# Kernel tuning notes

Measured on AMD Instinct MI355X. Metric: run time of the kernel, lower is better.

## Reference

```python
import jax, jax.numpy as jnp
import numpy as np

B, S, D = 8, 2048, 128
NEG = -1e9

def setup_inputs() -> dict:
    key = jax.random.key(0)
    kq, kk, kv = jax.random.split(key, 3)
    query = jax.random.normal(kq, (B, S, D), dtype=jnp.float32)
    k_ = jax.random.normal(kk, (B, S, D), dtype=jnp.float32)
    value = jax.random.normal(kv, (B, S, D), dtype=jnp.float32)
    mask = jnp.tril(jnp.ones((S, S), dtype=jnp.int32))  # causal (seq_len, seq_len)
    return {"query": query, "key": k_, "value": value, "mask": mask}

def reference(query, key, value, mask):
    d_k = query.shape[-1]
    # scores: [B, S, S]
    scores = jnp.einsum('bqd,bkd->bqk', query, key) / jnp.sqrt(jnp.asarray(d_k, jnp.float32))
    scores = jnp.where(mask == 0, jnp.asarray(NEG, scores.dtype), scores)
    p_attn = jax.nn.softmax(scores, axis=-1)
    # dropout p=0.0 -> identity
    return jnp.einsum('bqk,bkd->bqd', p_attn, value)
```

## Files before the change

kernel.cpp:

```cpp
#include <hip/hip_runtime.h>


#define BATCH 8
#define SEQ   2048
#define DIM   128
#define CK    256

typedef _Float16 v4h __attribute__((ext_vector_type(4)));
typedef _Float16 v8h __attribute__((ext_vector_type(8)));
typedef float    v4f __attribute__((ext_vector_type(4)));

#define QF_H 0u
#define KF_H 2097152u
#define VF_H 4194304u
#define OP_H 6291456u
#define ML_B 31457280u
#define WS_NEED 31752192u

__constant__ const float kScale = 0.08838834764831845f;

__global__ __launch_bounds__(256) void prepass(
    const float* __restrict__ K, const float* __restrict__ V,
    _Float16* __restrict__ wsh)
{
    const int b = blockIdx.x;
    const int t = threadIdx.x;
    if (b < 1024) {
        __shared__ float tile[16][132];
        const int batch = b >> 7, vt = b & 127;
        const float* src = V + ((size_t)batch * SEQ + vt * 16) * DIM;
        const int row = t >> 4, col = (t & 15) * 8;
        *(v4f*)&tile[row][col]     = *(const v4f*)(src + (size_t)row * DIM + col);
        *(v4f*)&tile[row][col + 4] = *(const v4f*)(src + (size_t)row * DIM + col + 4);
        __syncthreads();
        const int n = t >> 4, p = (t >> 2) & 3, qd = t & 3;
        v8h h;
        #pragma unroll
        for (int j = 0; j < 8; ++j) {
            const int d  = 32 * p + 16 * (j >> 2) + n;
            const int kk = qd * 4 + (j & 3);
            h[j] = (_Float16)tile[kk][d];
        }
        const int w = n * 64 + ((p * 16 + qd * 4) ^ ((n & 7) << 2));
        *(v8h*)(wsh + VF_H + (size_t)batch * 262144 + vt * 2048 + w * 2) = h;
    } else {
        const int i = (b - 1024) * 256 + t;
        const int seg = i & 15, row = i >> 4;
        const float* src = K + (size_t)row * DIM + seg * 8;
        v4f a = *(const v4f*)src;
        v4f c = *(const v4f*)(src + 4);
        v8h h;
        #pragma unroll
        for (int j = 0; j < 4; ++j) {
            h[j]     = (_Float16)a[j];
            h[j + 4] = (_Float16)c[j];
        }
        const int w = (seg * 4) ^ ((row & 7) << 2);
        *(v8h*)(wsh + KF_H + (size_t)row * DIM + w * 2) = h;
    }
}

__device__ __forceinline__ void dma16(const _Float16* g, const _Float16* l) {
    __builtin_amdgcn_global_load_lds(
        (const __attribute__((address_space(1))) unsigned int*)g,
        (__attribute__((address_space(3))) unsigned int*)(unsigned int)(uintptr_t)l,
        16, 0, 0);
}

__global__ __launch_bounds__(256, 4) void attn_chunk(
    const float* __restrict__ Q, const _Float16* __restrict__ wsh,
    float* __restrict__ Ml, _Float16* __restrict__ Op)
{
    __shared__ __align__(16) _Float16 lds[16384];

    const int batch = blockIdx.x & 7;
    int g = blockIdx.x >> 3;
    int c = 0;
    for (; c < 8; ++c) { const int cnt = 32 - 4 * c; if (g < cnt) break; g -= cnt; }
    const int wave = threadIdx.x >> 6;
    const int qt = 16 * c + g * 4 + wave;
    const int q0 = qt * 16;
    const int kbeg = c * CK;

    const int lane = threadIdx.x & 63;
    const int n = lane & 15, quad = lane >> 4;
    const size_t bo = (size_t)batch * SEQ * DIM;

    const _Float16* Kf = wsh + KF_H + bo;
    const _Float16* Vf = wsh + VF_H + bo;

    v8h qa[4];
    {
        const float* qp = Q + bo + (size_t)(q0 + n) * DIM + quad * 8;
        #pragma unroll
        for (int p = 0; p < 4; ++p) {
            v4f a = *(const v4f*)(qp + p * 32);
            v4f b2 = *(const v4f*)(qp + p * 32 + 4);
            v8h h;
            #pragma unroll
            for (int j = 0; j < 4; ++j) {
                h[j]     = (_Float16)(a[j] * kScale);
                h[j + 4] = (_Float16)(b2[j] * kScale);
            }
            qa[p] = h;
        }
    }

    const _Float16* gseg = ((wave < 2) ? (Kf + (size_t)kbeg * DIM)
                                       : (Vf + (size_t)(kbeg >> 4) * 2048))
                           + (wave & 1) * 2048;
    const int ldsseg = (wave >> 1) * 4096 + (wave & 1) * 2048;

    int koff[4];
    #pragma unroll
    for (int p = 0; p < 4; ++p)
        koff[p] = n * 128 + (((quad * 4 + p * 16) ^ ((n & 7) << 2)) << 1);

    float l_run = 0.0f;
    v4f of[8];
    #pragma unroll
    for (int dc = 0; dc < 8; ++dc) of[dc] = (v4f){0.f, 0.f, 0.f, 0.f};

    const int qn0 = q0 + n - kbeg;
    const int kq = quad * 4;

    #pragma unroll
    for (int i = 0; i < 4; ++i)
        dma16(gseg + i * 512 + lane * 8, &lds[ldsseg + i * 512]);

    #pragma unroll
    for (int kb = 0; kb < 8; ++kb) {
        __syncthreads();
        if (kb < 7) {
            const _Float16* gs = gseg + (kb + 1) * 4096;
            const int lb = ((kb + 1) & 1) * 8192 + ldsseg;
            #pragma unroll
            for (int i = 0; i < 4; ++i)
                dma16(gs + i * 512 + lane * 8, &lds[lb + i * 512]);
        }
        const int base = (kb & 1) * 8192;
        #pragma unroll
        for (int t16 = 0; t16 < 2; ++t16) {
            v4f s = (v4f){0.f, 0.f, 0.f, 0.f};
            #pragma unroll
            for (int p = 0; p < 4; ++p) {
                v8h kf = *(const v8h*)&lds[base + t16 * 2048 + koff[p]];
                s = __builtin_amdgcn_mfma_f32_16x16x32_f16(kf, qa[p], s, 0, 0, 0);
            }
            v4h pf;
            float ps = 0.f;
            #pragma unroll
            for (int r = 0; r < 4; ++r) {
                const float sv = (kb * 32 + t16 * 16 + kq + r > qn0) ? -1e30f : s[r];
                const float p = __expf(sv);
                ps += p;
                pf[r] = (_Float16)p;
            }
            l_run += ps;
            #pragma unroll
            for (int p = 0; p < 4; ++p) {
                v8h vv = *(const v8h*)&lds[base + 4096 + t16 * 2048 + koff[p]];
                v4h vlo = __builtin_shufflevector(vv, vv, 0, 1, 2, 3);
                v4h vhi = __builtin_shufflevector(vv, vv, 4, 5, 6, 7);
                of[2 * p]     = __builtin_amdgcn_mfma_f32_16x16x16f16(vlo, pf, of[2 * p], 0, 0, 0);
                of[2 * p + 1] = __builtin_amdgcn_mfma_f32_16x16x16f16(vhi, pf, of[2 * p + 1], 0, 0, 0);
            }
        }
    }

    l_run += __shfl_xor(l_run, 16);
    l_run += __shfl_xor(l_run, 32);

    const int rs = (2048 * c - 128 * c * (c - 1)) * 8
                 + batch * (2048 - CK * c) + (q0 + n - CK * c);
    _Float16* op = (_Float16*)(wsh + OP_H) + (size_t)rs * DIM
                 - (size_t)0;
    op = Op + (size_t)rs * DIM;
    #pragma unroll
    for (int dc = 0; dc < 8; ++dc) {
        v4h o;
        #pragma unroll
        for (int r = 0; r < 4; ++r) o[r] = (_Float16)of[dc][r];
        *(v4h*)(op + dc * 16 + quad * 4) = o;
    }
    if (quad == 0) Ml[rs] = l_run;
}

__global__ __launch_bounds__(256) void combine(
    const _Float16* __restrict__ Op, const float* __restrict__ Ml,
    float* __restrict__ O)
{
    const int gid = blockIdx.x * 256 + threadIdx.x;
    const size_t e = (size_t)gid * 4;
    const int d = (int)(e & 127);
    const int q = (int)((e >> 7) & 2047);
    const int b = (int)(e >> 18);
    const int nc = (q >> 8) + 1;
    float L = 0.f;
    v4f acc = (v4f){0.f, 0.f, 0.f, 0.f};
    for (int c = 0; c < nc; ++c) {
        const int rs = (2048 * c - 128 * c * (c - 1)) * 8 + b * (2048 - 256 * c) + (q - 256 * c);
        L += Ml[rs];
        v4h o = *(const v4h*)(Op + (size_t)rs * DIM + d);
        #pragma unroll
        for (int r = 0; r < 4; ++r) acc[r] += (float)o[r];
    }
    const float rl = 1.0f / L;
    *(v4f*)(O + e) = acc * rl;
}

__global__ __launch_bounds__(128) void attn_fwd(
    const float* __restrict__ Q, const float* __restrict__ K,
    const float* __restrict__ V, float* __restrict__ O)
{
    const int batch = blockIdx.x & 7;
    const int qb    = blockIdx.x >> 3;
    const int tid   = threadIdx.x;
    const int wave  = tid >> 6;
    const int lane  = tid & 63;
    const int n     = lane & 15;
    const int quad  = lane >> 4;

    const int q0      = qb * 32 + wave * 16;
    const int my_last = qb * 2 + wave;
    const int nt      = qb * 2 + 2;

    const size_t bo = (size_t)batch * SEQ * DIM;

    __shared__ __align__(16) _Float16 Ks[16 * 136];
    __shared__ __align__(16) _Float16 Vt[128 * 20];
    typedef _Float16 v2h __attribute__((ext_vector_type(2)));

    v4h qf[8];
    {
        const float* qp = Q + bo + (size_t)(q0 + n) * DIM + quad * 4;
        #pragma unroll
        for (int dc = 0; dc < 8; ++dc) {
            v4f qv = *(const v4f*)(qp + dc * 16);
            v4h h;
            #pragma unroll
            for (int i = 0; i < 4; ++i) h[i] = (_Float16)(qv[i] * kScale);
            qf[dc] = h;
        }
    }

    float m_run = -1e30f, l_run = 0.0f;
    v4f of[8];
    #pragma unroll
    for (int dc = 0; dc < 8; ++dc) of[dc] = (v4f){0.f, 0.f, 0.f, 0.f};

    const int krow = tid >> 3;
    const int kcol = (tid & 7) * 16;
    const int vr   = (tid >> 4) * 2;
    const int vc   = (tid & 15) * 4;

    for (int tk = 0; tk < nt; ++tk) {
        const int k0 = tk * 16;
        {
            const float* kp = K + bo + (size_t)(k0 + krow) * DIM + kcol;
            v4f k0v = *(const v4f*)(kp);
            v4f k1v = *(const v4f*)(kp + 4);
            v4f k2v = *(const v4f*)(kp + 8);
            v4f k3v = *(const v4f*)(kp + 12);
            const float* vp = V + bo + (size_t)(k0 + vr) * DIM + vc;
            v4f va0 = *(const v4f*)(vp);
            v4f va1 = *(const v4f*)(vp + DIM);
            v4f vb0 = *(const v4f*)(vp + 64);
            v4f vb1 = *(const v4f*)(vp + DIM + 64);

            v8h h0, h1;
            #pragma unroll
            for (int i = 0; i < 4; ++i) {
                h0[i]     = (_Float16)k0v[i];
                h0[i + 4] = (_Float16)k1v[i];
                h1[i]     = (_Float16)k2v[i];
                h1[i + 4] = (_Float16)k3v[i];
            }
            *(v8h*)&Ks[krow * 136 + kcol]     = h0;
            *(v8h*)&Ks[krow * 136 + kcol + 8] = h1;

            #pragma unroll
            for (int i = 0; i < 4; ++i) {
                v2h p0 = { (_Float16)va0[i], (_Float16)va1[i] };
                v2h p1 = { (_Float16)vb0[i], (_Float16)vb1[i] };
                *(v2h*)&Vt[(vc + i) * 20 + vr]      = p0;
                *(v2h*)&Vt[(vc + 64 + i) * 20 + vr] = p1;
            }
        }
        __syncthreads();

        if (tk <= my_last) {
            v4f s = (v4f){0.f, 0.f, 0.f, 0.f};
            #pragma unroll
            for (int dc = 0; dc < 8; ++dc) {
                v4h kf = *(const v4h*)&Ks[n * 136 + dc * 16 + quad * 4];
                s = __builtin_amdgcn_mfma_f32_16x16x16f16(kf, qf[dc], s, 0, 0, 0);
            }
            if (tk == my_last) {
                #pragma unroll
                for (int r = 0; r < 4; ++r)
                    if (quad * 4 + r > n) s[r] = -1e30f;
            }
            float tm = fmaxf(fmaxf(s[0], s[1]), fmaxf(s[2], s[3]));
            tm = fmaxf(tm, __shfl_xor(tm, 16));
            tm = fmaxf(tm, __shfl_xor(tm, 32));
            const float m_new = fmaxf(m_run, tm);
            const float alpha = __expf(m_run - m_new);
            v4f p;
            #pragma unroll
            for (int r = 0; r < 4; ++r) p[r] = __expf(s[r] - m_new);
            float ps = p[0] + p[1] + p[2] + p[3];
            ps += __shfl_xor(ps, 16);
            ps += __shfl_xor(ps, 32);
            l_run = l_run * alpha + ps;
            m_run = m_new;

            v4h pf;
            #pragma unroll
            for (int r = 0; r < 4; ++r) pf[r] = (_Float16)p[r];

            #pragma unroll
            for (int dc = 0; dc < 8; ++dc) {
                v4h vf = *(const v4h*)&Vt[(dc * 16 + n) * 20 + quad * 4];
                of[dc] *= alpha;
                of[dc] = __builtin_amdgcn_mfma_f32_16x16x16f16(vf, pf, of[dc], 0, 0, 0);
            }
        }
        __syncthreads();
    }

    const float rl = 1.0f / l_run;
    float* op = O + bo + (size_t)(q0 + n) * DIM + quad * 4;
    #pragma unroll
    for (int dc = 0; dc < 8; ++dc) {
        v4f o = of[dc] * rl;
        *(v4f*)(op + dc * 16) = o;
    }
}

extern "C" void kernel_launch(void* const* d_in, const int* in_sizes, int n_in,
                              void* d_out, int out_size, void* d_ws, size_t ws_size,
                              hipStream_t stream) {
    const float* Q = (const float*)d_in[0];
    const float* K = (const float*)d_in[1];
    const float* V = (const float*)d_in[2];
    float* Out = (float*)d_out;

    if (ws_size >= (size_t)WS_NEED) {
        _Float16* wsh = (_Float16*)d_ws;
        _Float16* Op  = wsh + OP_H;
        float*    Ml  = (float*)((char*)d_ws + ML_B);
        prepass<<<dim3(2048), dim3(256), 0, stream>>>(K, V, wsh);
        attn_chunk<<<dim3(8 * 144), dim3(256), 0, stream>>>(Q, wsh, Ml, Op);
        combine<<<dim3(2048), dim3(256), 0, stream>>>(Op, Ml, Out);
    } else {
        attn_fwd<<<dim3(BATCH * (SEQ / 32)), dim3(128), 0, stream>>>(Q, K, V, Out);
    }
}
```

Baseline: 112.0 us.

## Fuse combine into chunk kernel via atomic last-block reduction and exp2

```diff
diff --git a/kernel.cpp b/kernel.cpp
--- a/kernel.cpp
+++ b/kernel.cpp
@@ -10,21 +10,23 @@
 typedef _Float16 v8h __attribute__((ext_vector_type(8)));
 typedef float    v4f __attribute__((ext_vector_type(4)));
 
-#define QF_H 0u
 #define KF_H 2097152u
 #define VF_H 4194304u
 #define OP_H 6291456u
 #define ML_B 31457280u
-#define WS_NEED 31752192u
-
-__constant__ const float kScale = 0.08838834764831845f;
+#define CNT_B 31752192u
+#define WS_NEED 31753216u
+
+__constant__ const float kScaleE2 = 0.12751744462783346f;
+__constant__ const float kScale   = 0.08838834764831845f;
 
 __global__ __launch_bounds__(256) void prepass(
     const float* __restrict__ K, const float* __restrict__ V,
-    _Float16* __restrict__ wsh)
+    _Float16* __restrict__ wsh, int* __restrict__ cnt)
 {
     const int b = blockIdx.x;
     const int t = threadIdx.x;
+    if (b == 0) cnt[t] = 0;
     if (b < 1024) {
         __shared__ float tile[16][132];
         const int batch = b >> 7, vt = b & 127;
@@ -69,18 +71,22 @@
 
 __global__ __launch_bounds__(256, 4) void attn_chunk(
     const float* __restrict__ Q, const _Float16* __restrict__ wsh,
-    float* __restrict__ Ml, _Float16* __restrict__ Op)
+    float* __restrict__ Ml, _Float16* __restrict__ Op,
+    int* __restrict__ cnt, float* __restrict__ O)
 {
     __shared__ __align__(16) _Float16 lds[16384];
+    __shared__ int sOld;
 
     const int batch = blockIdx.x & 7;
     int g = blockIdx.x >> 3;
     int c = 0;
-    for (; c < 8; ++c) { const int cnt = 32 - 4 * c; if (g < cnt) break; g -= cnt; }
+    for (; c < 8; ++c) { const int n4 = 32 - 4 * c; if (g < n4) break; g -= n4; }
     const int wave = threadIdx.x >> 6;
     const int qt = 16 * c + g * 4 + wave;
     const int q0 = qt * 16;
     const int kbeg = c * CK;
+    const int J = 4 * c + g;
+    const int nc = (J >> 2) + 1;
 
     const int lane = threadIdx.x & 63;
     const int n = lane & 15, quad = lane >> 4;
@@ -99,8 +105,8 @@
             v8h h;
             #pragma unroll
             for (int j = 0; j < 4; ++j) {
-                h[j]     = (_Float16)(a[j] * kScale);
-                h[j + 4] = (_Float16)(b2[j] * kScale);
+                h[j]     = (_Float16)(a[j] * kScaleE2);
+                h[j + 4] = (_Float16)(b2[j] * kScaleE2);
             }
             qa[p] = h;
         }
@@ -152,7 +158,7 @@
             #pragma unroll
             for (int r = 0; r < 4; ++r) {
                 const float sv = (kb * 32 + t16 * 16 + kq + r > qn0) ? -1e30f : s[r];
-                const float p = __expf(sv);
+                const float p = exp2f(sv);
                 ps += p;
                 pf[r] = (_Float16)p;
             }
@@ -171,11 +177,18 @@
     l_run += __shfl_xor(l_run, 16);
     l_run += __shfl_xor(l_run, 32);
 
+    if (nc == 1) {
+        const float rl = 1.0f / l_run;
+        float* Of = O + bo + (size_t)(q0 + n) * DIM;
+        #pragma unroll
+        for (int dc = 0; dc < 8; ++dc)
+            *(v4f*)(Of + dc * 16 + quad * 4) = of[dc] * rl;
+        return;
+    }
+
     const int rs = (2048 * c - 128 * c * (c - 1)) * 8
                  + batch * (2048 - CK * c) + (q0 + n - CK * c);
-    _Float16* op = (_Float16*)(wsh + OP_H) + (size_t)rs * DIM
-                 - (size_t)0;
-    op = Op + (size_t)rs * DIM;
+    _Float16* op = Op + (size_t)rs * DIM;
     #pragma unroll
     for (int dc = 0; dc < 8; ++dc) {
         v4h o;
@@ -184,29 +197,40 @@
         *(v4h*)(op + dc * 16 + quad * 4) = o;
     }
     if (quad == 0) Ml[rs] = l_run;
-}
-
-__global__ __launch_bounds__(256) void combine(
-    const _Float16* __restrict__ Op, const float* __restrict__ Ml,
-    float* __restrict__ O)
-{
-    const int gid = blockIdx.x * 256 + threadIdx.x;
-    const size_t e = (size_t)gid * 4;
-    const int d = (int)(e & 127);
-    const int q = (int)((e >> 7) & 2047);
-    const int b = (int)(e >> 18);
-    const int nc = (q >> 8) + 1;
-    float L = 0.f;
-    v4f acc = (v4f){0.f, 0.f, 0.f, 0.f};
-    for (int c = 0; c < nc; ++c) {
-        const int rs = (2048 * c - 128 * c * (c - 1)) * 8 + b * (2048 - 256 * c) + (q - 256 * c);
-        L += Ml[rs];
-        v4h o = *(const v4h*)(Op + (size_t)rs * DIM + d);
-        #pragma unroll
-        for (int r = 0; r < 4; ++r) acc[r] += (float)o[r];
-    }
-    const float rl = 1.0f / L;
-    *(v4f*)(O + e) = acc * rl;
+
+    __threadfence();
+    __syncthreads();
+    if (threadIdx.x == 0) sOld = atomicAdd(&cnt[batch * 32 + J], 1);
+    __syncthreads();
+    if (sOld == nc - 1) {
+        __threadfence();
+        const int t = threadIdx.x;
+        const int q = 64 * J + (t >> 2);
+        const int dseg = (t & 3) * 32;
+        float acc[32];
+        #pragma unroll
+        for (int x = 0; x < 32; ++x) acc[x] = 0.f;
+        float L = 0.f;
+        for (int cc = 0; cc < nc; ++cc) {
+            const int rr = (2048 * cc - 128 * cc * (cc - 1)) * 8
+                         + batch * (2048 - CK * cc) + (q - CK * cc);
+            L += Ml[rr];
+            const _Float16* pp = Op + (size_t)rr * DIM + dseg;
+            #pragma unroll
+            for (int j = 0; j < 4; ++j) {
+                v8h h = *(const v8h*)(pp + j * 8);
+                #pragma unroll
+                for (int x = 0; x < 8; ++x) acc[j * 8 + x] += (float)h[x];
+            }
+        }
+        const float rl = 1.0f / L;
+        float* Of = O + bo + (size_t)q * DIM + dseg;
+        #pragma unroll
+        for (int j = 0; j < 8; ++j) {
+            v4f o = { acc[j*4] * rl, acc[j*4+1] * rl, acc[j*4+2] * rl, acc[j*4+3] * rl };
+            *(v4f*)(Of + j * 4) = o;
+        }
+    }
 }
 
 __global__ __launch_bounds__(128) void attn_fwd(
@@ -350,9 +374,9 @@
         _Float16* wsh = (_Float16*)d_ws;
         _Float16* Op  = wsh + OP_H;
         float*    Ml  = (float*)((char*)d_ws + ML_B);
-        prepass<<<dim3(2048), dim3(256), 0, stream>>>(K, V, wsh);
-        attn_chunk<<<dim3(8 * 144), dim3(256), 0, stream>>>(Q, wsh, Ml, Op);
-        combine<<<dim3(2048), dim3(256), 0, stream>>>(Op, Ml, Out);
+        int*      cnt = (int*)((char*)d_ws + CNT_B);
+        prepass<<<dim3(2048), dim3(256), 0, stream>>>(K, V, wsh, cnt);
+        attn_chunk<<<dim3(8 * 144), dim3(256), 0, stream>>>(Q, wsh, Ml, Op, cnt, Out);
     } else {
         attn_fwd<<<dim3(BATCH * (SEQ / 32)), dim3(128), 0, stream>>>(Q, K, V, Out);
     }
```

Result: slower. 287.6 us (+156.7%).

## Process two query tiles per wave and write single-chunk rows directly

Applied to the files above, without the earlier changes.

```diff
diff --git a/kernel.cpp b/kernel.cpp
--- a/kernel.cpp
+++ b/kernel.cpp
@@ -10,14 +10,14 @@
 typedef _Float16 v8h __attribute__((ext_vector_type(8)));
 typedef float    v4f __attribute__((ext_vector_type(4)));
 
-#define QF_H 0u
 #define KF_H 2097152u
 #define VF_H 4194304u
 #define OP_H 6291456u
 #define ML_B 31457280u
 #define WS_NEED 31752192u
 
-__constant__ const float kScale = 0.08838834764831845f;
+__constant__ const float kScaleE2 = 0.12751744462783346f;
+__constant__ const float kScale   = 0.08838834764831845f;
 
 __global__ __launch_bounds__(256) void prepass(
     const float* __restrict__ K, const float* __restrict__ V,
@@ -33,7 +33,7 @@
         *(v4f*)&tile[row][col]     = *(const v4f*)(src + (size_t)row * DIM + col);
         *(v4f*)&tile[row][col + 4] = *(const v4f*)(src + (size_t)row * DIM + col + 4);
         __syncthreads();
-        const int n = t >> 4, p = (t >> 2) & 3, qd = t & 3;
+        const int n = t & 15, p = (t >> 4) & 3, qd = t >> 6;
         v8h h;
         #pragma unroll
         for (int j = 0; j < 8; ++j) {
@@ -67,20 +67,23 @@
         16, 0, 0);
 }
 
-__global__ __launch_bounds__(256, 4) void attn_chunk(
+__global__ __launch_bounds__(256, 3) void attn_chunk(
     const float* __restrict__ Q, const _Float16* __restrict__ wsh,
-    float* __restrict__ Ml, _Float16* __restrict__ Op)
+    float* __restrict__ Ml, _Float16* __restrict__ Op,
+    float* __restrict__ O)
 {
     __shared__ __align__(16) _Float16 lds[16384];
 
     const int batch = blockIdx.x & 7;
     int g = blockIdx.x >> 3;
     int c = 0;
-    for (; c < 8; ++c) { const int cnt = 32 - 4 * c; if (g < cnt) break; g -= cnt; }
+    for (; c < 8; ++c) { const int n8 = 16 - 2 * c; if (g < n8) break; g -= n8; }
     const int wave = threadIdx.x >> 6;
-    const int qt = 16 * c + g * 4 + wave;
-    const int q0 = qt * 16;
+    const int qtb = 16 * c + g * 8;
+    const int q0a = (qtb + 2 * wave) * 16;
+    const int q0b = q0a + 16;
     const int kbeg = c * CK;
+    const bool direct = (c == 0) && (g < 2);
 
     const int lane = threadIdx.x & 63;
     const int n = lane & 15, quad = lane >> 4;
@@ -89,20 +92,26 @@
     const _Float16* Kf = wsh + KF_H + bo;
     const _Float16* Vf = wsh + VF_H + bo;
 
-    v8h qa[4];
+    v8h qa[8];
     {
-        const float* qp = Q + bo + (size_t)(q0 + n) * DIM + quad * 8;
+        const float* qpa = Q + bo + (size_t)(q0a + n) * DIM + quad * 8;
+        const float* qpb = Q + bo + (size_t)(q0b + n) * DIM + quad * 8;
         #pragma unroll
         for (int p = 0; p < 4; ++p) {
-            v4f a = *(const v4f*)(qp + p * 32);
-            v4f b2 = *(const v4f*)(qp + p * 32 + 4);
-            v8h h;
+            v4f a0 = *(const v4f*)(qpa + p * 32);
+            v4f a1 = *(const v4f*)(qpa + p * 32 + 4);
+            v4f b0 = *(const v4f*)(qpb + p * 32);
+            v4f b1 = *(const v4f*)(qpb + p * 32 + 4);
+            v8h ha, hb;
             #pragma unroll
             for (int j = 0; j < 4; ++j) {
-                h[j]     = (_Float16)(a[j] * kScale);
-                h[j + 4] = (_Float16)(b2[j] * kScale);
-            }
-            qa[p] = h;
+                ha[j]     = (_Float16)(a0[j] * kScaleE2);
+                ha[j + 4] = (_Float16)(a1[j] * kScaleE2);
+                hb[j]     = (_Float16)(b0[j] * kScaleE2);
+                hb[j + 4] = (_Float16)(b1[j] * kScaleE2);
+            }
+            qa[p]     = ha;
+            qa[4 + p] = hb;
         }
     }
 
@@ -116,12 +125,16 @@
     for (int p = 0; p < 4; ++p)
         koff[p] = n * 128 + (((quad * 4 + p * 16) ^ ((n & 7) << 2)) << 1);
 
-    float l_run = 0.0f;
-    v4f of[8];
-    #pragma unroll
-    for (int dc = 0; dc < 8; ++dc) of[dc] = (v4f){0.f, 0.f, 0.f, 0.f};
-
-    const int qn0 = q0 + n - kbeg;
+    float lA = 0.0f, lB = 0.0f;
+    v4f ofA[8], ofB[8];
+    #pragma unroll
+    for (int dc = 0; dc < 8; ++dc) {
+        ofA[dc] = (v4f){0.f, 0.f, 0.f, 0.f};
+        ofB[dc] = (v4f){0.f, 0.f, 0.f, 0.f};
+    }
+
+    const int qnA = q0a + n - kbeg;
+    const int qnB = qnA + 16;
     const int kq = quad * 4;
 
     #pragma unroll
@@ -141,49 +154,76 @@
         const int base = (kb & 1) * 8192;
         #pragma unroll
         for (int t16 = 0; t16 < 2; ++t16) {
-            v4f s = (v4f){0.f, 0.f, 0.f, 0.f};
+            v8h kf[4];
+            #pragma unroll
+            for (int p = 0; p < 4; ++p)
+                kf[p] = *(const v8h*)&lds[base + t16 * 2048 + koff[p]];
+            v4f sA = (v4f){0.f, 0.f, 0.f, 0.f};
+            v4f sB = (v4f){0.f, 0.f, 0.f, 0.f};
             #pragma unroll
             for (int p = 0; p < 4; ++p) {
-                v8h kf = *(const v8h*)&lds[base + t16 * 2048 + koff[p]];
-                s = __builtin_amdgcn_mfma_f32_16x16x32_f16(kf, qa[p], s, 0, 0, 0);
-            }
-            v4h pf;
-            float ps = 0.f;
+                sA = __builtin_amdgcn_mfma_f32_16x16x32_f16(kf[p], qa[p],     sA, 0, 0, 0);
+                sB = __builtin_amdgcn_mfma_f32_16x16x32_f16(kf[p], qa[4 + p], sB, 0, 0, 0);
+            }
+            const int kl = kb * 32 + t16 * 16 + kq;
+            v4h pfA, pfB;
+            float psA = 0.f, psB = 0.f;
             #pragma unroll
             for (int r = 0; r < 4; ++r) {
-                const float sv = (kb * 32 + t16 * 16 + kq + r > qn0) ? -1e30f : s[r];
-                const float p = __expf(sv);
-                ps += p;
-                pf[r] = (_Float16)p;
-            }
-            l_run += ps;
+                const float svA = (kl + r > qnA) ? -1e30f : sA[r];
+                const float svB = (kl + r > qnB) ? -1e30f : sB[r];
+                const float pA = exp2f(svA);
+                const float pB = exp2f(svB);
+                psA += pA; psB += pB;
+                pfA[r] = (_Float16)pA;
+                pfB[r] = (_Float16)pB;
+            }
+            lA += psA; lB += psB;
             #pragma unroll
             for (int p = 0; p < 4; ++p) {
                 v8h vv = *(const v8h*)&lds[base + 4096 + t16 * 2048 + koff[p]];
                 v4h vlo = __builtin_shufflevector(vv, vv, 0, 1, 2, 3);
                 v4h vhi = __builtin_shufflevector(vv, vv, 4, 5, 6, 7);
-                of[2 * p]     = __builtin_amdgcn_mfma_f32_16x16x16f16(vlo, pf, of[2 * p], 0, 0, 0);
-                of[2 * p + 1] = __builtin_amdgcn_mfma_f32_16x16x16f16(vhi, pf, of[2 * p + 1], 0, 0, 0);
-            }
-        }
-    }
-
-    l_run += __shfl_xor(l_run, 16);
-    l_run += __shfl_xor(l_run, 32);
-
-    const int rs = (2048 * c - 128 * c * (c - 1)) * 8
-                 + batch * (2048 - CK * c) + (q0 + n - CK * c);
-    _Float16* op = (_Float16*)(wsh + OP_H) + (size_t)rs * DIM
-                 - (size_t)0;
-    op = Op + (size_t)rs * DIM;
+                ofA[2*p]   = __builtin_amdgcn_mfma_f32_16x16x16f16(vlo, pfA, ofA[2*p],   0, 0, 0);
+                ofA[2*p+1] = __builtin_amdgcn_mfma_f32_16x16x16f16(vhi, pfA, ofA[2*p+1], 0, 0, 0);
+                ofB[2*p]   = __builtin_amdgcn_mfma_f32_16x16x16f16(vlo, pfB, ofB[2*p],   0, 0, 0);
+                ofB[2*p+1] = __builtin_amdgcn_mfma_f32_16x16x16f16(vhi, pfB, ofB[2*p+1], 0, 0, 0);
+            }
+        }
+    }
+
+    lA += __shfl_xor(lA, 16); lA += __shfl_xor(lA, 32);
+    lB += __shfl_xor(lB, 16); lB += __shfl_xor(lB, 32);
+
+    if (direct) {
+        const float rlA = 1.0f / lA, rlB = 1.0f / lB;
+        float* OfA = O + bo + (size_t)(q0a + n) * DIM;
+        float* OfB = O + bo + (size_t)(q0b + n) * DIM;
+        #pragma unroll
+        for (int dc = 0; dc < 8; ++dc) {
+            *(v4f*)(OfA + dc * 16 + quad * 4) = ofA[dc] * rlA;
+            *(v4f*)(OfB + dc * 16 + quad * 4) = ofB[dc] * rlB;
+        }
+        return;
+    }
+
+    const int rsA = (2048 * c - 128 * c * (c - 1)) * 8
+                  + batch * (2048 - CK * c) + (q0a + n - CK * c);
+    const int rsB = rsA + 16;
+    _Float16* opA = Op + (size_t)rsA * DIM;
+    _Float16* opB = Op + (size_t)rsB * DIM;
     #pragma unroll
     for (int dc = 0; dc < 8; ++dc) {
-        v4h o;
-        #pragma unroll
-        for (int r = 0; r < 4; ++r) o[r] = (_Float16)of[dc][r];
-        *(v4h*)(op + dc * 16 + quad * 4) = o;
-    }
-    if (quad == 0) Ml[rs] = l_run;
+        v4h oA, oB;
+        #pragma unroll
+        for (int r = 0; r < 4; ++r) {
+            oA[r] = (_Float16)ofA[dc][r];
+            oB[r] = (_Float16)ofB[dc][r];
+        }
+        *(v4h*)(opA + dc * 16 + quad * 4) = oA;
+        *(v4h*)(opB + dc * 16 + quad * 4) = oB;
+    }
+    if (quad == 0) { Ml[rsA] = lA; Ml[rsB] = lB; }
 }
 
 __global__ __launch_bounds__(256) void combine(
@@ -191,22 +231,28 @@
     float* __restrict__ O)
 {
     const int gid = blockIdx.x * 256 + threadIdx.x;
-    const size_t e = (size_t)gid * 4;
+    const size_t e = (size_t)gid * 8;
     const int d = (int)(e & 127);
     const int q = (int)((e >> 7) & 2047);
     const int b = (int)(e >> 18);
+    if (q < 256) return;
     const int nc = (q >> 8) + 1;
     float L = 0.f;
-    v4f acc = (v4f){0.f, 0.f, 0.f, 0.f};
+    float acc[8];
+    #pragma unroll
+    for (int x = 0; x < 8; ++x) acc[x] = 0.f;
     for (int c = 0; c < nc; ++c) {
         const int rs = (2048 * c - 128 * c * (c - 1)) * 8 + b * (2048 - 256 * c) + (q - 256 * c);
         L += Ml[rs];
-        v4h o = *(const v4h*)(Op + (size_t)rs * DIM + d);
-        #pragma unroll
-        for (int r = 0; r < 4; ++r) acc[r] += (float)o[r];
+        v8h o = *(const v8h*)(Op + (size_t)rs * DIM + d);
+        #pragma unroll
+        for (int x = 0; x < 8; ++x) acc[x] += (float)o[x];
     }
     const float rl = 1.0f / L;
-    *(v4f*)(O + e) = acc * rl;
+    v4f o0 = { acc[0] * rl, acc[1] * rl, acc[2] * rl, acc[3] * rl };
+    v4f o1 = { acc[4] * rl, acc[5] * rl, acc[6] * rl, acc[7] * rl };
+    *(v4f*)(O + e)     = o0;
+    *(v4f*)(O + e + 4) = o1;
 }
 
 __global__ __launch_bounds__(128) void attn_fwd(
@@ -351,8 +397,8 @@
         _Float16* Op  = wsh + OP_H;
         float*    Ml  = (float*)((char*)d_ws + ML_B);
         prepass<<<dim3(2048), dim3(256), 0, stream>>>(K, V, wsh);
-        attn_chunk<<<dim3(8 * 144), dim3(256), 0, stream>>>(Q, wsh, Ml, Op);
-        combine<<<dim3(2048), dim3(256), 0, stream>>>(Op, Ml, Out);
+        attn_chunk<<<dim3(8 * 72), dim3(256), 0, stream>>>(Q, wsh, Ml, Op, Out);
+        combine<<<dim3(1024), dim3(256), 0, stream>>>(Op, Ml, Out);
     } else {
         attn_fwd<<<dim3(BATCH * (SEQ / 32)), dim3(128), 0, stream>>>(Q, K, V, Out);
     }
```

Result: slower. 115.6 us (+3.2%).

## Write first-chunk rows directly, widen combine, use exp2 with folded scale

Applied to the files above, without the earlier changes.

```diff
diff --git a/kernel.cpp b/kernel.cpp
--- a/kernel.cpp
+++ b/kernel.cpp
@@ -10,14 +10,14 @@
 typedef _Float16 v8h __attribute__((ext_vector_type(8)));
 typedef float    v4f __attribute__((ext_vector_type(4)));
 
-#define QF_H 0u
-#define KF_H 2097152u
-#define VF_H 4194304u
-#define OP_H 6291456u
-#define ML_B 31457280u
-#define WS_NEED 31752192u
-
-__constant__ const float kScale = 0.08838834764831845f;
+#define KF_H 0u
+#define VF_H 2097152u
+#define OP_H 4194304u
+#define ML_B 27262976u
+#define WS_NEED 27557888u
+
+__constant__ const float kScaleE2 = 0.12751744462783346f;
+__constant__ const float kScale   = 0.08838834764831845f;
 
 __global__ __launch_bounds__(256) void prepass(
     const float* __restrict__ K, const float* __restrict__ V,
@@ -33,7 +33,7 @@
         *(v4f*)&tile[row][col]     = *(const v4f*)(src + (size_t)row * DIM + col);
         *(v4f*)&tile[row][col + 4] = *(const v4f*)(src + (size_t)row * DIM + col + 4);
         __syncthreads();
-        const int n = t >> 4, p = (t >> 2) & 3, qd = t & 3;
+        const int n = t & 15, p = (t >> 4) & 3, qd = t >> 6;
         v8h h;
         #pragma unroll
         for (int j = 0; j < 8; ++j) {
@@ -69,18 +69,20 @@
 
 __global__ __launch_bounds__(256, 4) void attn_chunk(
     const float* __restrict__ Q, const _Float16* __restrict__ wsh,
-    float* __restrict__ Ml, _Float16* __restrict__ Op)
+    float* __restrict__ Ml, _Float16* __restrict__ Op,
+    float* __restrict__ O)
 {
     __shared__ __align__(16) _Float16 lds[16384];
 
     const int batch = blockIdx.x & 7;
     int g = blockIdx.x >> 3;
     int c = 0;
-    for (; c < 8; ++c) { const int cnt = 32 - 4 * c; if (g < cnt) break; g -= cnt; }
+    for (; c < 8; ++c) { const int n4 = 32 - 4 * c; if (g < n4) break; g -= n4; }
     const int wave = threadIdx.x >> 6;
     const int qt = 16 * c + g * 4 + wave;
     const int q0 = qt * 16;
     const int kbeg = c * CK;
+    const bool direct = (c == 0) && (g < 4);
 
     const int lane = threadIdx.x & 63;
     const int n = lane & 15, quad = lane >> 4;
@@ -99,8 +101,8 @@
             v8h h;
             #pragma unroll
             for (int j = 0; j < 4; ++j) {
-                h[j]     = (_Float16)(a[j] * kScale);
-                h[j + 4] = (_Float16)(b2[j] * kScale);
+                h[j]     = (_Float16)(a[j] * kScaleE2);
+                h[j + 4] = (_Float16)(b2[j] * kScaleE2);
             }
             qa[p] = h;
         }
@@ -147,12 +149,13 @@
                 v8h kf = *(const v8h*)&lds[base + t16 * 2048 + koff[p]];
                 s = __builtin_amdgcn_mfma_f32_16x16x32_f16(kf, qa[p], s, 0, 0, 0);
             }
+            const int kl = kb * 32 + t16 * 16 + kq;
             v4h pf;
             float ps = 0.f;
             #pragma unroll
             for (int r = 0; r < 4; ++r) {
-                const float sv = (kb * 32 + t16 * 16 + kq + r > qn0) ? -1e30f : s[r];
-                const float p = __expf(sv);
+                const float sv = (kl + r > qn0) ? -1e30f : s[r];
+                const float p = exp2f(sv);
                 ps += p;
                 pf[r] = (_Float16)p;
             }
@@ -171,11 +174,18 @@
     l_run += __shfl_xor(l_run, 16);
     l_run += __shfl_xor(l_run, 32);
 
+    if (direct) {
+        const float rl = 1.0f / l_run;
+        float* Of = O + bo + (size_t)(q0 + n) * DIM;
+        #pragma unroll
+        for (int dc = 0; dc < 8; ++dc)
+            *(v4f*)(Of + dc * 16 + quad * 4) = of[dc] * rl;
+        return;
+    }
+
     const int rs = (2048 * c - 128 * c * (c - 1)) * 8
                  + batch * (2048 - CK * c) + (q0 + n - CK * c);
-    _Float16* op = (_Float16*)(wsh + OP_H) + (size_t)rs * DIM
-                 - (size_t)0;
-    op = Op + (size_t)rs * DIM;
+    _Float16* op = Op + (size_t)rs * DIM;
     #pragma unroll
     for (int dc = 0; dc < 8; ++dc) {
         v4h o;
@@ -191,22 +201,29 @@
     float* __restrict__ O)
 {
     const int gid = blockIdx.x * 256 + threadIdx.x;
-    const size_t e = (size_t)gid * 4;
+    const size_t e = (size_t)gid * 8;
     const int d = (int)(e & 127);
     const int q = (int)((e >> 7) & 2047);
     const int b = (int)(e >> 18);
+    if (q < CK) return;
     const int nc = (q >> 8) + 1;
     float L = 0.f;
-    v4f acc = (v4f){0.f, 0.f, 0.f, 0.f};
+    float acc[8];
+    #pragma unroll
+    for (int x = 0; x < 8; ++x) acc[x] = 0.f;
     for (int c = 0; c < nc; ++c) {
-        const int rs = (2048 * c - 128 * c * (c - 1)) * 8 + b * (2048 - 256 * c) + (q - 256 * c);
+        const int rs = (2048 * c - 128 * c * (c - 1)) * 8
+                     + b * (2048 - CK * c) + (q - CK * c);
         L += Ml[rs];
-        v4h o = *(const v4h*)(Op + (size_t)rs * DIM + d);
-        #pragma unroll
-        for (int r = 0; r < 4; ++r) acc[r] += (float)o[r];
+        v8h o = *(const v8h*)(Op + (size_t)rs * DIM + d);
+        #pragma unroll
+        for (int x = 0; x < 8; ++x) acc[x] += (float)o[x];
     }
     const float rl = 1.0f / L;
-    *(v4f*)(O + e) = acc * rl;
+    v4f o0 = { acc[0] * rl, acc[1] * rl, acc[2] * rl, acc[3] * rl };
+    v4f o1 = { acc[4] * rl, acc[5] * rl, acc[6] * rl, acc[7] * rl };
+    *(v4f*)(O + e)     = o0;
+    *(v4f*)(O + e + 4) = o1;
 }
 
 __global__ __launch_bounds__(128) void attn_fwd(
@@ -351,8 +368,8 @@
         _Float16* Op  = wsh + OP_H;
         float*    Ml  = (float*)((char*)d_ws + ML_B);
         prepass<<<dim3(2048), dim3(256), 0, stream>>>(K, V, wsh);
-        attn_chunk<<<dim3(8 * 144), dim3(256), 0, stream>>>(Q, wsh, Ml, Op);
-        combine<<<dim3(2048), dim3(256), 0, stream>>>(Op, Ml, Out);
+        attn_chunk<<<dim3(8 * 144), dim3(256), 0, stream>>>(Q, wsh, Ml, Op, Out);
+        combine<<<dim3(1024), dim3(256), 0, stream>>>(Op, Ml, Out);
     } else {
         attn_fwd<<<dim3(BATCH * (SEQ / 32)), dim3(128), 0, stream>>>(Q, K, V, Out);
     }
```

Result: slower. 114.8 us (+2.5%).
